# Performance work log

Measured on AMD Instinct MI355X. Metric: run time of the kernel, lower is better.

The kernel has to match this reference:

```python
import jax, jax.numpy as jnp
import numpy as np

B, T = 256, 2048
DIM_OUT, DIM_IN = 16, 16
H = 32  # hidden_size; 4H = 128 gates (i, f, g, o, PyTorch order)


def setup_inputs() -> dict:
    key = jax.random.key(0)
    ks = jax.random.split(key, 12)
    s = 1.0 / np.sqrt(H)  # PyTorch LSTM init scale
    return {
        "output_sequence": jax.random.normal(ks[0], (B, T, DIM_OUT), jnp.float32),
        "input_sequence": jax.random.normal(ks[1], (B, T, DIM_IN), jnp.float32),
        "W_ih0": jax.random.uniform(ks[2], (2, 4 * H, DIM_IN + DIM_OUT), jnp.float32, -s, s),
        "W_hh0": jax.random.uniform(ks[3], (2, 4 * H, H), jnp.float32, -s, s),
        "b_ih0": jax.random.uniform(ks[4], (2, 4 * H), jnp.float32, -s, s),
        "b_hh0": jax.random.uniform(ks[5], (2, 4 * H), jnp.float32, -s, s),
        "W_ih1": jax.random.uniform(ks[6], (2, 4 * H, 2 * H), jnp.float32, -s, s),
        "W_hh1": jax.random.uniform(ks[7], (2, 4 * H, H), jnp.float32, -s, s),
        "b_ih1": jax.random.uniform(ks[8], (2, 4 * H), jnp.float32, -s, s),
        "b_hh1": jax.random.uniform(ks[9], (2, 4 * H), jnp.float32, -s, s),
    }


def _lstm_dir(xg, W_hh, reverse):
    # xg: [T, B, 4H] precomputed input-side gate pre-activations (incl. both biases)
    def step(carry, g):
        h, c = carry
        g = g + h @ W_hh.T
        i, f, gg, o = jnp.split(g, 4, axis=-1)
        c = jax.nn.sigmoid(f) * c + jax.nn.sigmoid(i) * jnp.tanh(gg)
        h = jax.nn.sigmoid(o) * jnp.tanh(c)
        return (h, c), h

    h0 = jnp.zeros((xg.shape[1], W_hh.shape[1]), xg.dtype)
    _, hs = jax.lax.scan(step, (h0, h0), xg, reverse=reverse)
    return hs  # [T, B, H], aligned to original time indices


def _bilstm_layer(x, W_ih, W_hh, b_ih, b_hh):
    # x: [T, B, F]; W_ih: [2, 4H, F]; direction 0 = forward, 1 = backward
    xg_f = jnp.einsum('tbf,gf->tbg', x, W_ih[0]) + b_ih[0] + b_hh[0]
    xg_b = jnp.einsum('tbf,gf->tbg', x, W_ih[1]) + b_ih[1] + b_hh[1]
    hf = _lstm_dir(xg_f, W_hh[0], reverse=False)
    hb = _lstm_dir(xg_b, W_hh[1], reverse=True)
    return jnp.concatenate([hf, hb], axis=-1)  # [T, B, 2H]


def reference(output_sequence, input_sequence, W_ih0, W_hh0, b_ih0, b_hh0,
              W_ih1, W_hh1, b_ih1, b_hh1):
    # forward(): flip input_sequence along time, concat with output_sequence
    io = jnp.concatenate([output_sequence, input_sequence[:, ::-1, :]], axis=-1)
    x = jnp.transpose(io, (1, 0, 2))  # [T, B, F] time-major for scan
    h1 = _bilstm_layer(x, W_ih0, W_hh0, b_ih0, b_hh0)
    h2 = _bilstm_layer(h1, W_ih1, W_hh1, b_ih1, b_hh1)
    return jnp.transpose(h2, (1, 0, 2))  # [B, T, 2H]
```

## Files before the change

### kernel.cpp

```cpp
#include <hip/hip_runtime.h>


#define T_LEN 2048
#define BATCH 256
#define HID   32

__device__ __forceinline__ float frcp(float x) { return __builtin_amdgcn_rcpf(x); }
__device__ __forceinline__ float rdlane(float v, int k) {
    return __int_as_float(__builtin_amdgcn_readlane(__float_as_int(v), k));
}

template<int N>
__device__ __forceinline__ void load_row(float* dst, const float* __restrict__ src) {
#pragma unroll
    for (int i = 0; i < N / 4; ++i) {
        float4 v = reinterpret_cast<const float4*>(src)[i];
        dst[4*i+0] = v.x; dst[4*i+1] = v.y; dst[4*i+2] = v.z; dst[4*i+3] = v.w;
    }
}

template<int LAYER>
__global__ __launch_bounds__(256) void xg_gemm_chunk(
        const float* __restrict__ OS, const float* __restrict__ IS,
        const float* __restrict__ h1,
        const float* __restrict__ Wih, const float* __restrict__ bih,
        const float* __restrict__ bhh, float* __restrict__ xg,
        int t_base, int C)
{
    constexpr int F  = (LAYER == 0) ? 32 : 64;
    constexpr int TT = 16;
    __shared__ float xs[2][TT][F];
    const int tid = threadIdx.x;
    const int d   = tid >> 7;
    const int g   = tid & 127;
    const int lt0 = blockIdx.x * TT;
    const int b   = blockIdx.y;

    constexpr int TOT = 2 * TT * F;
#pragma unroll
    for (int rep = 0; rep < TOT / 256; ++rep) {
        int flat = rep * 256 + tid;
        int d2  = flat / (TT * F);
        int rem = flat % (TT * F);
        int tt  = rem / F, f = rem % F;
        int tl  = t_base + lt0 + tt;
        int te  = d2 ? (T_LEN - 1 - tl) : tl;
        float v;
        if (LAYER == 0) {
            v = (f < 16) ? OS[((size_t)b * T_LEN + te) * 16 + f]
                         : IS[((size_t)b * T_LEN + (T_LEN - 1 - te)) * 16 + (f - 16)];
        } else {
            v = h1[((size_t)te * BATCH + b) * 64 + f];
        }
        xs[d2][tt][f] = v;
    }

    float w[F];
    load_row<F>(w, Wih + ((size_t)d * 128 + g) * F);
    const float bias = bih[d * 128 + g] + bhh[d * 128 + g];
    __syncthreads();

#pragma unroll
    for (int tt = 0; tt < TT; ++tt) {
        float a0 = bias, a1 = 0.f, a2 = 0.f, a3 = 0.f;
#pragma unroll
        for (int j = 0; j < F / 4; ++j) {
            float4 x = reinterpret_cast<const float4*>(xs[d][tt])[j];
            a0 = fmaf(x.x, w[4*j+0], a0);
            a1 = fmaf(x.y, w[4*j+1], a1);
            a2 = fmaf(x.z, w[4*j+2], a2);
            a3 = fmaf(x.w, w[4*j+3], a3);
        }
        xg[(((size_t)d * C + (lt0 + tt)) * BATCH + b) * 128 + g] = (a0 + a1) + (a2 + a3);
    }
}

template<int LAYER>
__global__ __launch_bounds__(64, 1) void lstm_rec_chunk(
        const float* __restrict__ xg, const float* __restrict__ Whh,
        float* __restrict__ outp, float* __restrict__ state,
        int t_base, int C)
{
    const int l   = threadIdx.x;
    const int b   = blockIdx.x;
    const int d   = blockIdx.y;
    const int gA  = l;
    const int gB  = 64 + l;
    const bool lo = (l < HID);
    const int chain = d * BATCH + b;

    float whh_a[HID], whh_b[HID];
    load_row<HID>(whh_a, Whh + ((size_t)d * 128 + gA) * HID);
    load_row<HID>(whh_b, Whh + ((size_t)d * 128 + gB) * HID);

    float c = 0.f, hj = 0.f;
    if (t_base > 0 && lo) {
        c  = state[(size_t)chain * 64 + l];
        hj = state[(size_t)chain * 64 + 32 + l];
    }
    float h[HID];
#pragma unroll
    for (int k = 0; k < HID; ++k) h[k] = rdlane(hj, k);

    const float* xgd = xg + ((size_t)d * C * BATCH + b) * 128;
    const size_t STRIDE = (size_t)BATCH * 128;

    constexpr int PF = 8;
    float ra[PF], rb[PF];
#pragma unroll
    for (int u = 0; u < PF; ++u) {
        ra[u] = xgd[(size_t)u * STRIDE + gA];
        rb[u] = xgd[(size_t)u * STRIDE + gB];
    }

#pragma unroll 1
    for (int tb = 0; tb < C; tb += PF) {
#pragma unroll
        for (int u = 0; u < PF; ++u) {
            const int lt = tb + u;
            const int tl = t_base + lt;
            const int te = d ? (T_LEN - 1 - tl) : tl;
            const float xa = ra[u], xb = rb[u];
            int tp = lt + PF; if (tp > C - 1) tp = C - 1;
            ra[u] = xgd[(size_t)tp * STRIDE + gA];
            rb[u] = xgd[(size_t)tp * STRIDE + gB];
            float a0 = xa, a1 = 0.f, a2 = 0.f, a3 = 0.f;
            float b0 = xb, b1 = 0.f, b2 = 0.f, b3 = 0.f;
#pragma unroll
            for (int k = 0; k < 8; ++k) {
                a0 = fmaf(h[k],      whh_a[k],      a0);
                a1 = fmaf(h[k + 8],  whh_a[k + 8],  a1);
                a2 = fmaf(h[k + 16], whh_a[k + 16], a2);
                a3 = fmaf(h[k + 24], whh_a[k + 24], a3);
                b0 = fmaf(h[k],      whh_b[k],      b0);
                b1 = fmaf(h[k + 8],  whh_b[k + 8],  b1);
                b2 = fmaf(h[k + 16], whh_b[k + 16], b2);
                b3 = fmaf(h[k + 24], whh_b[k + 24], b3);
            }
            const float accA = (a0 + a1) + (a2 + a3);
            const float accB = (b0 + b1) + (b2 + b3);
            float sA = frcp(1.f + __expf(-accA));
            float argB = lo ? (-2.f * accB) : (-accB);
            float rB = frcp(1.f + __expf(argB));
            float sB = lo ? fmaf(2.f, rB, -1.f) : rB;
            float sf = __shfl(sA, (l + 32) & 63);
            float so = __shfl(sB, (l + 32) & 63);
            c = fmaf(sf, c, sA * sB);
            float tc = fmaf(2.f, frcp(1.f + __expf(-2.f * c)), -1.f);
            hj = so * tc;
            if (lo) {
                if constexpr (LAYER == 0)
                    outp[((size_t)te * BATCH + b) * 64 + d * HID + l] = hj;
                else
                    outp[((size_t)b * T_LEN + te) * 64 + d * HID + l] = hj;
            }
#pragma unroll
            for (int k = 0; k < HID; ++k) h[k] = rdlane(hj, k);
        }
    }

    if (lo) {
        state[(size_t)chain * 64 + l]      = c;
        state[(size_t)chain * 64 + 32 + l] = hj;
    }
}

template<int LAYER>
__global__ __launch_bounds__(64, 1) void lstm_rec(
        const float* __restrict__ OS, const float* __restrict__ IS,
        const float* __restrict__ Wih, const float* __restrict__ Whh,
        const float* __restrict__ bih, const float* __restrict__ bhh,
        const float* __restrict__ h1in, float* __restrict__ outp)
{
    constexpr int F = (LAYER == 0) ? 32 : 64;
    const int l   = threadIdx.x;
    const int b   = blockIdx.x;
    const int dir = blockIdx.y;
    const int gA  = l;
    const int gB  = 64 + l;

    float wih_a[F], wih_b[F], whh_a[HID], whh_b[HID];
    load_row<F>(wih_a, Wih + ((size_t)dir * 128 + gA) * F);
    load_row<F>(wih_b, Wih + ((size_t)dir * 128 + gB) * F);
    load_row<HID>(whh_a, Whh + ((size_t)dir * 128 + gA) * HID);
    load_row<HID>(whh_b, Whh + ((size_t)dir * 128 + gB) * HID);
    const float biasA = bih[dir * 128 + gA] + bhh[dir * 128 + gA];
    const float biasB = bih[dir * 128 + gB] + bhh[dir * 128 + gB];

    float h[HID];
#pragma unroll
    for (int k = 0; k < HID; ++k) h[k] = 0.f;
    float c = 0.f;
    const bool lo = (l < HID);

    float4 X0[F / 4], X1[F / 4];

    auto load_x = [&](float4* X, int tl) {
        const int te = dir ? (T_LEN - 1 - tl) : tl;
        if constexpr (LAYER == 0) {
            const float4* p0 = reinterpret_cast<const float4*>(OS + ((size_t)b * T_LEN + te) * 16);
            const float4* p1 = reinterpret_cast<const float4*>(IS + ((size_t)b * T_LEN + (T_LEN - 1 - te)) * 16);
#pragma unroll
            for (int i = 0; i < 4; ++i) X[i] = p0[i];
#pragma unroll
            for (int i = 0; i < 4; ++i) X[4 + i] = p1[i];
        } else {
            const float4* p = reinterpret_cast<const float4*>(h1in + ((size_t)te * BATCH + b) * 64);
#pragma unroll
            for (int i = 0; i < F / 4; ++i) X[i] = p[i];
        }
    };

    auto step = [&](int tl, const float4* X) {
        const int te = dir ? (T_LEN - 1 - tl) : tl;
        float accA = biasA, accB = biasB;
#pragma unroll
        for (int i = 0; i < F / 4; ++i) {
            accA = fmaf(X[i].x, wih_a[4*i+0], accA);
            accA = fmaf(X[i].y, wih_a[4*i+1], accA);
            accA = fmaf(X[i].z, wih_a[4*i+2], accA);
            accA = fmaf(X[i].w, wih_a[4*i+3], accA);
            accB = fmaf(X[i].x, wih_b[4*i+0], accB);
            accB = fmaf(X[i].y, wih_b[4*i+1], accB);
            accB = fmaf(X[i].z, wih_b[4*i+2], accB);
            accB = fmaf(X[i].w, wih_b[4*i+3], accB);
        }
#pragma unroll
        for (int k = 0; k < HID; ++k) {
            accA = fmaf(h[k], whh_a[k], accA);
            accB = fmaf(h[k], whh_b[k], accB);
        }
        float sA = frcp(1.f + __expf(-accA));
        float argB = lo ? (-2.f * accB) : (-accB);
        float rB = frcp(1.f + __expf(argB));
        float sB = lo ? fmaf(2.f, rB, -1.f) : rB;
        float sf = __shfl(sA, (l + 32) & 63);
        float so = __shfl(sB, (l + 32) & 63);
        c = fmaf(sf, c, sA * sB);
        float tc = fmaf(2.f, frcp(1.f + __expf(-2.f * c)), -1.f);
        float hj = so * tc;
        if (lo) {
            if constexpr (LAYER == 0)
                outp[((size_t)te * BATCH + b) * 64 + dir * HID + l] = hj;
            else
                outp[((size_t)b * T_LEN + te) * 64 + dir * HID + l] = hj;
        }
#pragma unroll
        for (int k = 0; k < HID; ++k) h[k] = rdlane(hj, k);
    };

    load_x(X0, 0);
#pragma unroll 1
    for (int tt = 0; tt < T_LEN; tt += 2) {
        load_x(X1, tt + 1);
        step(tt, X0);
        int nx = tt + 2; if (nx > T_LEN - 1) nx = T_LEN - 1;
        load_x(X0, nx);
        step(tt + 1, X1);
    }
}

extern "C" void kernel_launch(void* const* d_in, const int* in_sizes, int n_in,
                              void* d_out, int out_size, void* d_ws, size_t ws_size,
                              hipStream_t stream) {
    const float* OS    = (const float*)d_in[0];
    const float* IS    = (const float*)d_in[1];
    const float* W_ih0 = (const float*)d_in[2];
    const float* W_hh0 = (const float*)d_in[3];
    const float* b_ih0 = (const float*)d_in[4];
    const float* b_hh0 = (const float*)d_in[5];
    const float* W_ih1 = (const float*)d_in[6];
    const float* W_hh1 = (const float*)d_in[7];
    const float* b_ih1 = (const float*)d_in[8];
    const float* b_hh1 = (const float*)d_in[9];
    float* out = (float*)d_out;

    const size_t H1_BYTES = (size_t)T_LEN * BATCH * 64 * sizeof(float);
    const size_t ST_BYTES = (size_t)512 * 64 * sizeof(float);

    int C = 0;
    if (ws_size > H1_BYTES + ST_BYTES) {
        size_t avail = ws_size - H1_BYTES - ST_BYTES;
        for (int nc = 1; nc <= 32; nc <<= 1) {
            size_t xg_bytes = (size_t)2 * (T_LEN / nc) * BATCH * 128 * sizeof(float);
            if (xg_bytes <= avail) { C = T_LEN / nc; break; }
        }
    }

    if (C >= 64) {
        float* h1 = (float*)d_ws;
        float* st = (float*)((char*)d_ws + H1_BYTES);
        float* xg = (float*)((char*)d_ws + H1_BYTES + ST_BYTES);
        dim3 gb(256), rb(64), rg(BATCH, 2);
        for (int t_base = 0; t_base < T_LEN; t_base += C) {
            dim3 gg(C / 16, BATCH);
            hipLaunchKernelGGL((xg_gemm_chunk<0>), gg, gb, 0, stream,
                               OS, IS, (const float*)nullptr, W_ih0, b_ih0, b_hh0, xg, t_base, C);
            hipLaunchKernelGGL((lstm_rec_chunk<0>), rg, rb, 0, stream,
                               xg, W_hh0, h1, st, t_base, C);
        }
        for (int t_base = 0; t_base < T_LEN; t_base += C) {
            dim3 gg(C / 16, BATCH);
            hipLaunchKernelGGL((xg_gemm_chunk<1>), gg, gb, 0, stream,
                               (const float*)nullptr, (const float*)nullptr, h1,
                               W_ih1, b_ih1, b_hh1, xg, t_base, C);
            hipLaunchKernelGGL((lstm_rec_chunk<1>), rg, rb, 0, stream,
                               xg, W_hh1, out, st, t_base, C);
        }
    } else {
        float* h1 = (float*)d_ws;
        dim3 grid(BATCH, 2), block(64);
        hipLaunchKernelGGL((lstm_rec<0>), grid, block, 0, stream,
                           OS, IS, W_ih0, W_hh0, b_ih0, b_hh0, (const float*)nullptr, h1);
        hipLaunchKernelGGL((lstm_rec<1>), grid, block, 0, stream,
                           (const float*)nullptr, (const float*)nullptr,
                           W_ih1, W_hh1, b_ih1, b_hh1, (const float*)h1, out);
    }
}
```

Baseline: 2.241 ms.

## Interleave both LSTM directions per wavefront with LDS h broadcast and packed FMA

The recurrent kernel now runs the forward and backward chains for one batch row inside a single 64-lane wavefront and alternates their steps, so one chain's latency can hide behind the other's. The grid shrinks from 512 to 256 blocks. The hidden state is broadcast through a double-buffered LDS array read as float4, replacing 32 readlanes per step, and the dot products use packed float2 FMAs. The cost is roughly double the register footprint for weights and prefetch buffers, plus extra workspace slack because the prefetch can now read past the end of a chunk.

```diff
diff --git a/kernel.cpp b/kernel.cpp
--- a/kernel.cpp
+++ b/kernel.cpp
@@ -4,6 +4,9 @@
 #define T_LEN 2048
 #define BATCH 256
 #define HID   32
+#define PF    8
+
+typedef __attribute__((ext_vector_type(2))) float f2;
 
 __device__ __forceinline__ float frcp(float x) { return __builtin_amdgcn_rcpf(x); }
 __device__ __forceinline__ float rdlane(float v, int k) {
@@ -16,6 +19,17 @@
     for (int i = 0; i < N / 4; ++i) {
         float4 v = reinterpret_cast<const float4*>(src)[i];
         dst[4*i+0] = v.x; dst[4*i+1] = v.y; dst[4*i+2] = v.z; dst[4*i+3] = v.w;
+    }
+}
+
+__device__ __forceinline__ void load_row_f2_32(f2* dst, const float* __restrict__ src) {
+#pragma unroll
+    for (int i = 0; i < 8; ++i) {
+        float4 v = reinterpret_cast<const float4*>(src)[i];
+        f2 a; a.x = v.x; a.y = v.y;
+        f2 b; b.x = v.z; b.y = v.w;
+        dst[2*i]   = a;
+        dst[2*i+1] = b;
     }
 }
 
@@ -76,92 +90,165 @@
 }
 
 template<int LAYER>
-__global__ __launch_bounds__(64, 1) void lstm_rec_chunk(
+__global__ __launch_bounds__(64, 1) void lstm_rec2(
         const float* __restrict__ xg, const float* __restrict__ Whh,
         float* __restrict__ outp, float* __restrict__ state,
         int t_base, int C)
 {
     const int l   = threadIdx.x;
     const int b   = blockIdx.x;
-    const int d   = blockIdx.y;
-    const int gA  = l;
-    const int gB  = 64 + l;
     const bool lo = (l < HID);
-    const int chain = d * BATCH + b;
-
-    float whh_a[HID], whh_b[HID];
-    load_row<HID>(whh_a, Whh + ((size_t)d * 128 + gA) * HID);
-    load_row<HID>(whh_b, Whh + ((size_t)d * 128 + gB) * HID);
-
-    float c = 0.f, hj = 0.f;
+    const int xl  = (l + 32) & 63;
+
+    const float mB = lo ? -2.f : -1.f;
+    const float kM = lo ?  2.f :  1.f;
+    const float kA = lo ? -1.f :  0.f;
+
+    f2 wA0[16], wB0[16], wA1[16], wB1[16];
+    load_row_f2_32(wA0, Whh + ((size_t)0 * 128 + l) * HID);
+    load_row_f2_32(wB0, Whh + ((size_t)0 * 128 + 64 + l) * HID);
+    load_row_f2_32(wA1, Whh + ((size_t)1 * 128 + l) * HID);
+    load_row_f2_32(wB1, Whh + ((size_t)1 * 128 + 64 + l) * HID);
+
+    float c0 = 0.f, h0j = 0.f, c1 = 0.f, h1j = 0.f;
     if (t_base > 0 && lo) {
-        c  = state[(size_t)chain * 64 + l];
-        hj = state[(size_t)chain * 64 + 32 + l];
-    }
-    float h[HID];
-#pragma unroll
-    for (int k = 0; k < HID; ++k) h[k] = rdlane(hj, k);
-
-    const float* xgd = xg + ((size_t)d * C * BATCH + b) * 128;
+        c0  = state[(size_t)(0 * BATCH + b) * 64 + l];
+        h0j = state[(size_t)(0 * BATCH + b) * 64 + 32 + l];
+        c1  = state[(size_t)(1 * BATCH + b) * 64 + l];
+        h1j = state[(size_t)(1 * BATCH + b) * 64 + 32 + l];
+    }
+
+    __shared__ __align__(16) float hbuf[2][2][HID];
+    if (lo) { hbuf[0][0][l] = h0j; hbuf[0][1][l] = h1j; }
+
     const size_t STRIDE = (size_t)BATCH * 128;
-
-    constexpr int PF = 8;
-    float ra[PF], rb[PF];
+    const float* xp0 = xg + (size_t)b * 128;
+    const float* xp1 = xg + (size_t)C * STRIDE + (size_t)b * 128;
+    const float* pf0 = xp0 + (size_t)PF * STRIDE;
+    const float* pf1 = xp1 + (size_t)PF * STRIDE;
+
+    float ra0[PF], rb0[PF], ra1[PF], rb1[PF];
 #pragma unroll
     for (int u = 0; u < PF; ++u) {
-        ra[u] = xgd[(size_t)u * STRIDE + gA];
-        rb[u] = xgd[(size_t)u * STRIDE + gB];
+        ra0[u] = xp0[(size_t)u * STRIDE + l];
+        rb0[u] = xp0[(size_t)u * STRIDE + 64 + l];
+        ra1[u] = xp1[(size_t)u * STRIDE + l];
+        rb1[u] = xp1[(size_t)u * STRIDE + 64 + l];
+    }
+
+    float *op0, *op1;
+    ptrdiff_t os0, os1;
+    {
+        const int teF = t_base;
+        const int teB = T_LEN - 1 - t_base;
+        if constexpr (LAYER == 0) {
+            op0 = outp + ((size_t)teF * BATCH + b) * 64 + 0 * HID + l;
+            op1 = outp + ((size_t)teB * BATCH + b) * 64 + 1 * HID + l;
+            os0 =  (ptrdiff_t)(BATCH * 64);
+            os1 = -(ptrdiff_t)(BATCH * 64);
+        } else {
+            op0 = outp + ((size_t)b * T_LEN + teF) * 64 + 0 * HID + l;
+            op1 = outp + ((size_t)b * T_LEN + teB) * 64 + 1 * HID + l;
+            os0 =  (ptrdiff_t)64;
+            os1 = -(ptrdiff_t)64;
+        }
     }
 
 #pragma unroll 1
     for (int tb = 0; tb < C; tb += PF) {
 #pragma unroll
+        for (int k = 0; k < 16; k += 4) {
+            asm volatile("" : "+v"(wA0[k]), "+v"(wA0[k+1]), "+v"(wA0[k+2]), "+v"(wA0[k+3]));
+            asm volatile("" : "+v"(wB0[k]), "+v"(wB0[k+1]), "+v"(wB0[k+2]), "+v"(wB0[k+3]));
+            asm volatile("" : "+v"(wA1[k]), "+v"(wA1[k+1]), "+v"(wA1[k+2]), "+v"(wA1[k+3]));
+            asm volatile("" : "+v"(wB1[k]), "+v"(wB1[k+1]), "+v"(wB1[k+2]), "+v"(wB1[k+3]));
+        }
+
+#pragma unroll
         for (int u = 0; u < PF; ++u) {
-            const int lt = tb + u;
-            const int tl = t_base + lt;
-            const int te = d ? (T_LEN - 1 - tl) : tl;
-            const float xa = ra[u], xb = rb[u];
-            int tp = lt + PF; if (tp > C - 1) tp = C - 1;
-            ra[u] = xgd[(size_t)tp * STRIDE + gA];
-            rb[u] = xgd[(size_t)tp * STRIDE + gB];
-            float a0 = xa, a1 = 0.f, a2 = 0.f, a3 = 0.f;
-            float b0 = xb, b1 = 0.f, b2 = 0.f, b3 = 0.f;
-#pragma unroll
-            for (int k = 0; k < 8; ++k) {
-                a0 = fmaf(h[k],      whh_a[k],      a0);
-                a1 = fmaf(h[k + 8],  whh_a[k + 8],  a1);
-                a2 = fmaf(h[k + 16], whh_a[k + 16], a2);
-                a3 = fmaf(h[k + 24], whh_a[k + 24], a3);
-                b0 = fmaf(h[k],      whh_b[k],      b0);
-                b1 = fmaf(h[k + 8],  whh_b[k + 8],  b1);
-                b2 = fmaf(h[k + 16], whh_b[k + 16], b2);
-                b3 = fmaf(h[k + 24], whh_b[k + 24], b3);
+            const int p = u & 1;
+            const float xa0 = ra0[u], xb0 = rb0[u];
+            const float xa1 = ra1[u], xb1 = rb1[u];
+            ra0[u] = pf0[l]; rb0[u] = pf0[64 + l]; pf0 += STRIDE;
+            ra1[u] = pf1[l]; rb1[u] = pf1[64 + l]; pf1 += STRIDE;
+
+            {
+                f2 h2[16];
+                const float4* hb = reinterpret_cast<const float4*>(&hbuf[p][0][0]);
+#pragma unroll
+                for (int r = 0; r < 8; ++r) {
+                    float4 q = hb[r];
+                    f2 a; a.x = q.x; a.y = q.y;
+                    f2 bb; bb.x = q.z; bb.y = q.w;
+                    h2[2*r] = a; h2[2*r+1] = bb;
+                }
+                f2 aA[4], aB[4];
+#pragma unroll
+                for (int j = 0; j < 4; ++j) { aA[j] = (f2)(0.f); aB[j] = (f2)(0.f); }
+#pragma unroll
+                for (int k = 0; k < 16; ++k) {
+                    aA[k & 3] = __builtin_elementwise_fma(h2[k], wA0[k], aA[k & 3]);
+                    aB[k & 3] = __builtin_elementwise_fma(h2[k], wB0[k], aB[k & 3]);
+                }
+                f2 sA2 = (aA[0] + aA[1]) + (aA[2] + aA[3]);
+                f2 sB2 = (aB[0] + aB[1]) + (aB[2] + aB[3]);
+                const float accA = xa0 + sA2.x + sA2.y;
+                const float accB = xb0 + sB2.x + sB2.y;
+
+                const float sA = frcp(1.f + __expf(-accA));
+                const float rB = frcp(1.f + __expf(mB * accB));
+                const float sB = fmaf(kM, rB, kA);
+                const float sf = __shfl(sA, xl);
+                const float so = __shfl(sB, xl);
+                c0 = fmaf(sf, c0, sA * sB);
+                const float tc = fmaf(2.f, frcp(1.f + __expf(-2.f * c0)), -1.f);
+                h0j = so * tc;
+                if (lo) { *op0 = h0j; hbuf[p ^ 1][0][l] = h0j; }
+                op0 += os0;
             }
-            const float accA = (a0 + a1) + (a2 + a3);
-            const float accB = (b0 + b1) + (b2 + b3);
-            float sA = frcp(1.f + __expf(-accA));
-            float argB = lo ? (-2.f * accB) : (-accB);
-            float rB = frcp(1.f + __expf(argB));
-            float sB = lo ? fmaf(2.f, rB, -1.f) : rB;
-            float sf = __shfl(sA, (l + 32) & 63);
-            float so = __shfl(sB, (l + 32) & 63);
-            c = fmaf(sf, c, sA * sB);
-            float tc = fmaf(2.f, frcp(1.f + __expf(-2.f * c)), -1.f);
-            hj = so * tc;
-            if (lo) {
-                if constexpr (LAYER == 0)
-                    outp[((size_t)te * BATCH + b) * 64 + d * HID + l] = hj;
-                else
-                    outp[((size_t)b * T_LEN + te) * 64 + d * HID + l] = hj;
+
+            {
+                f2 h2[16];
+                const float4* hb = reinterpret_cast<const float4*>(&hbuf[p][1][0]);
+#pragma unroll
+                for (int r = 0; r < 8; ++r) {
+                    float4 q = hb[r];
+                    f2 a; a.x = q.x; a.y = q.y;
+                    f2 bb; bb.x = q.z; bb.y = q.w;
+                    h2[2*r] = a; h2[2*r+1] = bb;
+                }
+                f2 aA[4], aB[4];
+#pragma unroll
+                for (int j = 0; j < 4; ++j) { aA[j] = (f2)(0.f); aB[j] = (f2)(0.f); }
+#pragma unroll
+                for (int k = 0; k < 16; ++k) {
+                    aA[k & 3] = __builtin_elementwise_fma(h2[k], wA1[k], aA[k & 3]);
+                    aB[k & 3] = __builtin_elementwise_fma(h2[k], wB1[k], aB[k & 3]);
+                }
+                f2 sA2 = (aA[0] + aA[1]) + (aA[2] + aA[3]);
+                f2 sB2 = (aB[0] + aB[1]) + (aB[2] + aB[3]);
+                const float accA = xa1 + sA2.x + sA2.y;
+                const float accB = xb1 + sB2.x + sB2.y;
+
+                const float sA = frcp(1.f + __expf(-accA));
+                const float rB = frcp(1.f + __expf(mB * accB));
+                const float sB = fmaf(kM, rB, kA);
+                const float sf = __shfl(sA, xl);
+                const float so = __shfl(sB, xl);
+                c1 = fmaf(sf, c1, sA * sB);
+                const float tc = fmaf(2.f, frcp(1.f + __expf(-2.f * c1)), -1.f);
+                h1j = so * tc;
+                if (lo) { *op1 = h1j; hbuf[p ^ 1][1][l] = h1j; }
+                op1 += os1;
             }
-#pragma unroll
-            for (int k = 0; k < HID; ++k) h[k] = rdlane(hj, k);
         }
     }
 
     if (lo) {
-        state[(size_t)chain * 64 + l]      = c;
-        state[(size_t)chain * 64 + 32 + l] = hj;
+        state[(size_t)(0 * BATCH + b) * 64 + l]      = c0;
+        state[(size_t)(0 * BATCH + b) * 64 + 32 + l] = h0j;
+        state[(size_t)(1 * BATCH + b) * 64 + l]      = c1;
+        state[(size_t)(1 * BATCH + b) * 64 + 32 + l] = h1j;
     }
 }
 
@@ -277,10 +364,11 @@
 
     const size_t H1_BYTES = (size_t)T_LEN * BATCH * 64 * sizeof(float);
     const size_t ST_BYTES = (size_t)512 * 64 * sizeof(float);
+    const size_t SLACK    = (size_t)PF * BATCH * 128 * sizeof(float);
 
     int C = 0;
-    if (ws_size > H1_BYTES + ST_BYTES) {
-        size_t avail = ws_size - H1_BYTES - ST_BYTES;
+    if (ws_size > H1_BYTES + ST_BYTES + SLACK) {
+        size_t avail = ws_size - H1_BYTES - ST_BYTES - SLACK;
         for (int nc = 1; nc <= 32; nc <<= 1) {
             size_t xg_bytes = (size_t)2 * (T_LEN / nc) * BATCH * 128 * sizeof(float);
             if (xg_bytes <= avail) { C = T_LEN / nc; break; }
@@ -291,12 +379,12 @@
         float* h1 = (float*)d_ws;
         float* st = (float*)((char*)d_ws + H1_BYTES);
         float* xg = (float*)((char*)d_ws + H1_BYTES + ST_BYTES);
-        dim3 gb(256), rb(64), rg(BATCH, 2);
+        dim3 gb(256), rb(64), rg(BATCH);
         for (int t_base = 0; t_base < T_LEN; t_base += C) {
             dim3 gg(C / 16, BATCH);
             hipLaunchKernelGGL((xg_gemm_chunk<0>), gg, gb, 0, stream,
                                OS, IS, (const float*)nullptr, W_ih0, b_ih0, b_hh0, xg, t_base, C);
-            hipLaunchKernelGGL((lstm_rec_chunk<0>), rg, rb, 0, stream,
+            hipLaunchKernelGGL((lstm_rec2<0>), rg, rb, 0, stream,
                                xg, W_hh0, h1, st, t_base, C);
         }
         for (int t_base = 0; t_base < T_LEN; t_base += C) {
@@ -304,7 +392,7 @@
             hipLaunchKernelGGL((xg_gemm_chunk<1>), gg, gb, 0, stream,
                                (const float*)nullptr, (const float*)nullptr, h1,
                                W_ih1, b_ih1, b_hh1, xg, t_base, C);
-            hipLaunchKernelGGL((lstm_rec_chunk<1>), rg, rb, 0, stream,
+            hipLaunchKernelGGL((lstm_rec2<1>), rg, rb, 0, stream,
                                xg, W_hh1, out, st, t_base, C);
         }
     } else {
```

New measurement: 2.716 ms. 21.2% more time.
